# Kernel optimization log

Hardware: AMD Instinct MI355X
Metric: run time of the kernel (lower is better)

## Reference

```python
import jax, jax.numpy as jnp
import numpy as np

B, S, D = 4, 1024, 4096
HQ, HKV, HD = 32, 8, 128
N_REP = HQ // HKV


def _rope(x, cos, sin):
    # x: [b, s, h, hd]; cos/sin: [s, hd//2]; pairs are (x[..., 2i], x[..., 2i+1])
    xr = x[..., 0::2]
    xi = x[..., 1::2]
    c = cos[None, :, None, :]
    s = sin[None, :, None, :]
    out_r = xr * c - xi * s
    out_i = xr * s + xi * c
    return jnp.stack([out_r, out_i], axis=-1).reshape(x.shape)


def setup_inputs() -> dict:
    key = jax.random.key(0)
    ks = jax.random.split(key, 6)
    x = jax.random.normal(ks[0], (B, S, D), dtype=jnp.float32)
    wq = jax.random.normal(ks[1], (HQ * HD, D), dtype=jnp.float32) * 0.02
    wk = jax.random.normal(ks[2], (HKV * HD, D), dtype=jnp.float32) * 0.02
    wv = jax.random.normal(ks[3], (HKV * HD, D), dtype=jnp.float32) * 0.02
    wo = jax.random.normal(ks[4], (D, HQ * HD), dtype=jnp.float32) * 0.02
    # standard rotary frequencies, theta=10000
    inv_freq = 1.0 / (10000.0 ** (np.arange(0, HD, 2, dtype=np.float32) / HD))
    angles = np.outer(np.arange(S, dtype=np.float32), inv_freq)  # [S, HD//2]
    freqs_cos = jnp.asarray(np.cos(angles), dtype=jnp.float32)
    freqs_sin = jnp.asarray(np.sin(angles), dtype=jnp.float32)
    cache_k = jnp.zeros((B, S, HKV, HD), dtype=jnp.float32)
    cache_v = jnp.zeros((B, S, HKV, HD), dtype=jnp.float32)
    return {"x": x, "wq": wq, "wk": wk, "wv": wv, "wo": wo,
            "freqs_cos": freqs_cos, "freqs_sin": freqs_sin,
            "cache_k": cache_k, "cache_v": cache_v, "start_pos": 0}


def reference(x, wq, wk, wv, wo, freqs_cos, freqs_sin, cache_k, cache_v, start_pos):
    b, s, _ = x.shape
    xq = jnp.einsum('bsd,od->bso', x, wq).reshape(b, s, HQ, HD)
    xk = jnp.einsum('bsd,od->bso', x, wk).reshape(b, s, HKV, HD)
    xv = jnp.einsum('bsd,od->bso', x, wv).reshape(b, s, HKV, HD)
    xq = _rope(xq, freqs_cos, freqs_sin)
    xk = _rope(xk, freqs_cos, freqs_sin)
    # KV-cache append (intended semantics: store keys/values)
    cache_k = jax.lax.dynamic_update_slice(cache_k, xk, (0, start_pos, 0, 0))
    cache_v = jax.lax.dynamic_update_slice(cache_v, xv, (0, start_pos, 0, 0))
    keys = cache_k[:, :start_pos + s]      # [b, kv, HKV, HD]
    values = cache_v[:, :start_pos + s]
    # GQA repeat_kv -> [b, kv, HQ, HD]
    keys = jnp.repeat(keys, N_REP, axis=2)
    values = jnp.repeat(values, N_REP, axis=2)
    scores = jnp.einsum('bqhd,bkhd->bhqk', xq, keys) / jnp.sqrt(jnp.float32(HD))
    probs = jax.nn.softmax(scores.astype(jnp.float32), axis=-1).astype(xq.dtype)
    out = jnp.einsum('bhqk,bkhd->bqhd', probs, values).reshape(b, s, HQ * HD)
    return jnp.einsum('bso,do->bsd', out, wo)
```

## Files before the change

kernel.cpp:

```cpp
#include <hip/hip_runtime.h>

typedef __bf16 bf16_t;
typedef __bf16 bf16x8 __attribute__((ext_vector_type(8)));
typedef __bf16 bf16x4 __attribute__((ext_vector_type(4)));
typedef float  f32x4  __attribute__((ext_vector_type(4)));
typedef short  s16x4  __attribute__((ext_vector_type(4)));

#define SEQ    1024
#define DMODEL 4096
#define NHQ    32
#define NHKV   8
#define HDIM   128

#define GLOAD_LDS16(g, l)                                                  \
    __builtin_amdgcn_global_load_lds(                                      \
        (const __attribute__((address_space(1))) unsigned int*)(g),        \
        (__attribute__((address_space(3))) unsigned int*)(l), 16, 0, 0)

__global__ __launch_bounds__(256)
void f2b(const float* __restrict__ in, bf16_t* __restrict__ out, int n8)
{
    int i = blockIdx.x * 256 + threadIdx.x;
    if (i >= n8) return;
    const float4* p = (const float4*)in + 2 * (size_t)i;
    float4 a = p[0], b = p[1];
    bf16x8 o;
    o[0] = (bf16_t)a.x; o[1] = (bf16_t)a.y; o[2] = (bf16_t)a.z; o[3] = (bf16_t)a.w;
    o[4] = (bf16_t)b.x; o[5] = (bf16_t)b.y; o[6] = (bf16_t)b.z; o[7] = (bf16_t)b.w;
    *((bf16x8*)out + i) = o;
}

#define STAGE_A(b, ks)  do {                                               \
    const char* as_ = Ab + (size_t)srow * Krb + (ks) + scol0;              \
    GLOAD_LDS16(as_,             ldsA[b] + t * 16);                        \
    GLOAD_LDS16(as_ + 128 * Krb, ldsA[b] + 8192 + t * 16);                 \
} while (0)
#define STAGE_B(b, ks)  do {                                               \
    const char* bs_ = Bb + (size_t)srow * Krb + (ks) + scol0;              \
    GLOAD_LDS16(bs_,             ldsB[b] + t * 16);                        \
    GLOAD_LDS16(bs_ + 128 * Krb, ldsB[b] + 8192 + t * 16);                 \
} while (0)
#define LDS_AT(buf, row, lg_) \
    (*(const bf16x8*)((buf) + (row) * 64 + (((lg_) * 16) ^ ((((row) >> 1) & 3) << 4))))

#define TILE(bufi, tno)  do {                                              \
    const int ks3_ = ((tno) + 3 < NT) ? ((tno) + 3) * 64 : 0;              \
      \
    bf16x8 af[8], bfr0, bfr1;                                              \
    _Pragma("unroll")                                                      \
    for (int m = 0; m < 8; ++m) {                                          \
        int row = wm * 128 + m * 16 + l15;                                 \
        af[m] = LDS_AT(ldsA[bufi], row, lg);                               \
    }                                                                      \
    { int rb = wn * 64 + l15;      bfr0 = LDS_AT(ldsB[bufi], rb, lg); }    \
    { int rb = wn * 64 + 16 + l15; bfr1 = LDS_AT(ldsB[bufi], rb, lg); }    \
    STAGE_A(((tno) + 3) & 3, ks3_);                                        \
    __builtin_amdgcn_sched_barrier(0);                                     \
    __builtin_amdgcn_s_barrier();                                          \
    asm volatile("s_waitcnt lgkmcnt(0)" ::: "memory");                     \
    __builtin_amdgcn_sched_barrier(0);                                     \
    __builtin_amdgcn_s_setprio(1);                                         \
    _Pragma("unroll")                                                      \
    for (int m = 0; m < 8; ++m) {                                          \
        acc[m][0] = __builtin_amdgcn_mfma_f32_16x16x32_bf16(af[m], bfr0, acc[m][0], 0, 0, 0); \
        acc[m][1] = __builtin_amdgcn_mfma_f32_16x16x32_bf16(af[m], bfr1, acc[m][1], 0, 0, 0); \
    }                                                                      \
    __builtin_amdgcn_s_setprio(0);                                         \
    __builtin_amdgcn_sched_barrier(0);                                     \
    __builtin_amdgcn_s_barrier();                                          \
       \
    { int rb = wn * 64 + 32 + l15; bfr0 = LDS_AT(ldsB[bufi], rb, lg); }    \
    { int rb = wn * 64 + 48 + l15; bfr1 = LDS_AT(ldsB[bufi], rb, lg); }    \
    STAGE_B(((tno) + 3) & 3, ks3_);                                        \
    __builtin_amdgcn_sched_barrier(0);                                     \
    __builtin_amdgcn_s_barrier();                                          \
    asm volatile("s_waitcnt lgkmcnt(0)" ::: "memory");                     \
    __builtin_amdgcn_sched_barrier(0);                                     \
    __builtin_amdgcn_s_setprio(1);                                         \
    _Pragma("unroll")                                                      \
    for (int m = 0; m < 8; ++m) {                                          \
        acc[m][2] = __builtin_amdgcn_mfma_f32_16x16x32_bf16(af[m], bfr0, acc[m][2], 0, 0, 0); \
        acc[m][3] = __builtin_amdgcn_mfma_f32_16x16x32_bf16(af[m], bfr1, acc[m][3], 0, 0, 0); \
    }                                                                      \
    __builtin_amdgcn_s_setprio(0);                                         \
    asm volatile("s_waitcnt vmcnt(8)" ::: "memory");                       \
    __builtin_amdgcn_sched_barrier(0);                                     \
    __builtin_amdgcn_s_barrier();                                          \
} while (0)

template<bool OUT_F32>
__global__ __launch_bounds__(512, 2)
void gemm256(const bf16_t* __restrict__ A, const bf16_t* __restrict__ B,
             void* __restrict__ Cv, int M, int N, int K, int nbn)
{
    __shared__ __align__(16) char ldsA[4][16384];
    __shared__ __align__(16) char ldsB[4][16384];

    const int nwg = gridDim.x;
    const int bid0 = blockIdx.x;
    const int bid = (bid0 & 7) * (nwg >> 3) + (bid0 >> 3);
    const int bm = bid / nbn, bn = bid % nbn;
    const int t = threadIdx.x;
    const int lane = t & 63, wid = t >> 6;
    const int wm = wid >> 2, wn = wid & 3;
    const int l15 = lane & 15, lg = lane >> 4;
    const int m0 = bm * 256, n0 = bn * 256;

    const int srow = t >> 2;
    const int scol0 = (((t & 3) ^ ((srow >> 1) & 3)) << 4);
    const int Krb = K * 2;
    const char* Ab = (const char*)A + (size_t)m0 * Krb;
    const char* Bb = (const char*)B + (size_t)n0 * Krb;

    const int NT = K >> 5;
    f32x4 acc[8][4] = {};

    STAGE_A(0, 0);   STAGE_B(0, 0);
    STAGE_A(1, 64);  STAGE_B(1, 64);
    STAGE_A(2, 128); STAGE_B(2, 128);
    asm volatile("s_waitcnt vmcnt(8)" ::: "memory");
    __builtin_amdgcn_sched_barrier(0);
    __builtin_amdgcn_s_barrier();

    for (int tt = 0; tt < NT; tt += 4) {
        TILE(0, tt + 0);
        TILE(1, tt + 1);
        TILE(2, tt + 2);
        TILE(3, tt + 3);
    }

    #pragma unroll
    for (int m = 0; m < 8; ++m) {
        int row0 = m0 + wm * 128 + m * 16 + lg * 4;
        #pragma unroll
        for (int n = 0; n < 4; ++n) {
            int col = n0 + wn * 64 + n * 16 + l15;
            #pragma unroll
            for (int i = 0; i < 4; ++i) {
                if constexpr (OUT_F32)
                    ((float*)Cv)[(size_t)(row0 + i) * N + col] = acc[m][n][i];
                else
                    ((bf16_t*)Cv)[(size_t)(row0 + i) * N + col] = (bf16_t)acc[m][n][i];
            }
        }
    }
}
#undef TILE
#undef LDS_AT
#undef STAGE_A
#undef STAGE_B

template<int MODE>
__global__ __launch_bounds__(256, 4)
void gemm_bt(const bf16_t* __restrict__ A, const bf16_t* __restrict__ B,
             void* __restrict__ Cv, bf16_t* __restrict__ Vt,
             int M, int N, int K, int nbn)
{
    __shared__ __align__(16) bf16_t lA[128 * 32];
    __shared__ __align__(16) bf16_t lB[128 * 32];

    const int nwg = gridDim.x;
    const int bid0 = blockIdx.x;
    const int bid = (bid0 & 7) * (nwg >> 3) + (bid0 >> 3);
    const int bm = bid / nbn, bn = bid % nbn;
    const int t = threadIdx.x;
    const int lane = t & 63, wid = t >> 6;
    const int wrow = (wid >> 1) * 64, wcol = (wid & 1) * 64;
    const int l15 = lane & 15, lg = lane >> 4;
    const int m0 = bm * 128, n0 = bn * 128;

    const int r0 = t >> 2, pos0 = (t & 3) * 8;
    const int r1 = r0 + 64;

    const bf16_t* Ar0 = A + (size_t)(m0 + r0) * K + pos0;
    const bf16_t* Ar1 = A + (size_t)(m0 + r1) * K + pos0;
    const bf16_t* Br0 = B + (size_t)(n0 + r0) * K + pos0;
    const bf16_t* Br1 = B + (size_t)(n0 + r1) * K + pos0;

    f32x4 acc[4][4] = {};

    for (int k0 = 0; k0 < K; k0 += 32) {
        __syncthreads();
        GLOAD_LDS16(Ar0 + k0, lA + t * 8);
        GLOAD_LDS16(Ar1 + k0, lA + (t + 256) * 8);
        GLOAD_LDS16(Br0 + k0, lB + t * 8);
        GLOAD_LDS16(Br1 + k0, lB + (t + 256) * 8);
        __syncthreads();

        bf16x8 af[4], bfr[4];
        #pragma unroll
        for (int m = 0; m < 4; ++m)
            af[m] = *(const bf16x8*)(lA + (wrow + m * 16 + l15) * 32 + lg * 8);
        #pragma unroll
        for (int n = 0; n < 4; ++n)
            bfr[n] = *(const bf16x8*)(lB + (wcol + n * 16 + l15) * 32 + lg * 8);
        #pragma unroll
        for (int m = 0; m < 4; ++m)
            #pragma unroll
            for (int n = 0; n < 4; ++n)
                acc[m][n] = __builtin_amdgcn_mfma_f32_16x16x32_bf16(
                    af[m], bfr[n], acc[m][n], 0, 0, 0);
    }

    #pragma unroll
    for (int m = 0; m < 4; ++m) {
        #pragma unroll
        for (int n = 0; n < 4; ++n) {
            int col  = n0 + wcol + n * 16 + l15;
            int row0 = m0 + wrow + m * 16 + lg * 4;
            if constexpr (MODE == 0) {
                #pragma unroll
                for (int i = 0; i < 4; ++i)
                    ((bf16_t*)Cv)[(size_t)(row0 + i) * N + col] = (bf16_t)acc[m][n][i];
            } else if constexpr (MODE == 1) {
                #pragma unroll
                for (int i = 0; i < 4; ++i)
                    ((float*)Cv)[(size_t)(row0 + i) * N + col] = acc[m][n][i];
            } else {
                if (col < 1024) {
                    #pragma unroll
                    for (int i = 0; i < 4; ++i)
                        ((bf16_t*)Cv)[(size_t)(row0 + i) * 1024 + col] = (bf16_t)acc[m][n][i];
                } else {
                    bf16x4 pk;
                    #pragma unroll
                    for (int i = 0; i < 4; ++i) pk[i] = (bf16_t)acc[m][n][i];
                    *(bf16x4*)(Vt + (size_t)(col - 1024) * 4096 + row0) = pk;
                }
            }
        }
    }
}

__global__ __launch_bounds__(256)
void rope_kernel(bf16_t* __restrict__ X, const float* __restrict__ fc,
                 const float* __restrict__ fs, int nheads, int rowstride)
{
    int idx = blockIdx.x * 256 + threadIdx.x;
    int j4 = idx & 15;
    int rest = idx >> 4;
    int h = rest % nheads;
    int tok = rest / nheads;
    int s = tok & (SEQ - 1);
    bf16_t* p = X + (size_t)tok * rowstride + h * HDIM + j4 * 8;
    bf16x8 v = *(const bf16x8*)p;
    float4 c  = *(const float4*)(fc + s * 64 + j4 * 4);
    float4 sn = *(const float4*)(fs + s * 64 + j4 * 4);
    bf16x8 o;
    o[0] = (bf16_t)((float)v[0] * c.x - (float)v[1] * sn.x);
    o[1] = (bf16_t)((float)v[0] * sn.x + (float)v[1] * c.x);
    o[2] = (bf16_t)((float)v[2] * c.y - (float)v[3] * sn.y);
    o[3] = (bf16_t)((float)v[2] * sn.y + (float)v[3] * c.y);
    o[4] = (bf16_t)((float)v[4] * c.z - (float)v[5] * sn.z);
    o[5] = (bf16_t)((float)v[4] * sn.z + (float)v[5] * c.z);
    o[6] = (bf16_t)((float)v[6] * c.w - (float)v[7] * sn.w);
    o[7] = (bf16_t)((float)v[6] * sn.w + (float)v[7] * c.w);
    *(bf16x8*)p = o;
}

__global__ __launch_bounds__(256, 4)
void attn_kernel(const bf16_t* __restrict__ Q, const bf16_t* __restrict__ Kg,
                 const bf16_t* __restrict__ Vtg, bf16_t* __restrict__ O)
{
    __shared__ __align__(16) char klds[64 * 256];
    __shared__ __align__(16) char vlds[128 * 128];

    const int nwg = gridDim.x;
    const int bid0 = blockIdx.x;
    const int blk = (bid0 & 7) * (nwg >> 3) + (bid0 >> 3);
    const int qt = blk & 15;
    const int bh = blk >> 4;
    const int b = bh >> 5, h = bh & 31, kv = h >> 2;
    const int t = threadIdx.x, lane = t & 63, wid = t >> 6;
    const int l15 = lane & 15, lg = lane >> 4;
    const int swzk = (l15 & 7) << 4;

    const float SCL = 0.08838834764831845f;
    const float L2E = 1.4426950408889634f;

    const int qrow = qt * 64 + wid * 16 + l15;
    const size_t qbase = (size_t)(b * SEQ + qrow) * DMODEL + h * HDIM;
    bf16x8 qf[4];
    #pragma unroll
    for (int dc = 0; dc < 4; ++dc)
        qf[dc] = *(const bf16x8*)(Q + qbase + dc * 32 + lg * 8);

    const char* kgb = (const char*)Kg + ((size_t)(b * SEQ) * 1024 + kv * HDIM) * 2;
    const char* vgb = (const char*)Vtg + ((size_t)(kv * HDIM) * 4096 + b * SEQ) * 2;

    f32x4 o[8] = {};
    float mrun = -3.0e38f, lrun = 0.f;

    for (int kt = 0; kt < 16; ++kt) {
        __syncthreads();
        #pragma unroll
        for (int i = 0; i < 4; ++i) {
            int idx = t + 256 * i;
            {
                int r = idx >> 4, cb = (idx & 15) << 4;
                const char* src = kgb + (size_t)(kt * 64 + r) * 2048
                                      + (cb ^ ((r & 7) << 4));
                GLOAD_LDS16(src, klds + idx * 16);
            }
            {
                int d = idx >> 3, cb = (idx & 7) << 4;
                const char* src = vgb + (size_t)d * 8192 + kt * 128
                                      + (cb ^ ((d & 7) << 4));
                GLOAD_LDS16(src, vlds + idx * 16);
            }
        }
        __syncthreads();

        f32x4 sacc[4] = {};
        #pragma unroll
        for (int kb = 0; kb < 4; ++kb) {
            const char* krow = klds + (kb * 16 + l15) * 256;
            #pragma unroll
            for (int dc = 0; dc < 4; ++dc) {
                bf16x8 kf = *(const bf16x8*)(krow + ((dc * 64 + lg * 16) ^ swzk));
                sacc[kb] = __builtin_amdgcn_mfma_f32_16x16x32_bf16(
                    kf, qf[dc], sacc[kb], 0, 0, 0);
            }
        }

        float sv[16];
        float mt = -3.0e38f;
        #pragma unroll
        for (int kb = 0; kb < 4; ++kb)
            #pragma unroll
            for (int i = 0; i < 4; ++i) {
                float s = sacc[kb][i] * SCL;
                sv[kb * 4 + i] = s;
                mt = fmaxf(mt, s);
            }
        mt = fmaxf(mt, __shfl_xor(mt, 16));
        mt = fmaxf(mt, __shfl_xor(mt, 32));
        float mnew = fmaxf(mrun, mt);
        float alpha = exp2f((mrun - mnew) * L2E);

        float ts = 0.f;
        s16x4 pf[4];
        #pragma unroll
        for (int kb = 0; kb < 4; ++kb)
            #pragma unroll
            for (int i = 0; i < 4; ++i) {
                float p = exp2f((sv[kb * 4 + i] - mnew) * L2E);
                ts += p;
                pf[kb][i] = (short)__builtin_bit_cast(unsigned short, (bf16_t)p);
            }
        ts += __shfl_xor(ts, 16);
        ts += __shfl_xor(ts, 32);
        lrun = lrun * alpha + ts;
        mrun = mnew;

        #pragma unroll
        for (int i = 0; i < 4; ++i) {
            float ai = __shfl(alpha, lg * 4 + i);
            #pragma unroll
            for (int db = 0; db < 8; ++db) o[db][i] *= ai;
        }

        #pragma unroll
        for (int kb = 0; kb < 4; ++kb)
            #pragma unroll
            for (int db = 0; db < 8; ++db) {
                int d = l15 + 16 * db;
                const char* va = vlds + d * 128 + ((kb * 32 + lg * 8) ^ swzk);
                s16x4 vf = *(const s16x4*)va;
                o[db] = __builtin_amdgcn_mfma_f32_16x16x16bf16_1k(
                    pf[kb], vf, o[db], 0, 0, 0);
            }
    }

    #pragma unroll
    for (int i = 0; i < 4; ++i) {
        float li = __shfl(lrun, lg * 4 + i);
        float inv = 1.0f / li;
        int row = b * SEQ + qt * 64 + wid * 16 + lg * 4 + i;
        #pragma unroll
        for (int db = 0; db < 8; ++db) {
            int col = h * HDIM + l15 + 16 * db;
            O[(size_t)row * DMODEL + col] = (bf16_t)(o[db][i] * inv);
        }
    }
}

extern "C" void kernel_launch(void* const* d_in, const int* in_sizes, int n_in,
                              void* d_out, int out_size, void* d_ws, size_t ws_size,
                              hipStream_t stream)
{
    const float* x  = (const float*)d_in[0];
    const float* wq = (const float*)d_in[1];
    const float* wk = (const float*)d_in[2];
    const float* wv = (const float*)d_in[3];
    const float* wo = (const float*)d_in[4];
    const float* fc = (const float*)d_in[5];
    const float* fs = (const float*)d_in[6];

    const size_t T = (size_t)4096;
    bf16_t* Qw   = (bf16_t*)d_ws;
    bf16_t* Kw2  = Qw   + T * 4096;
    bf16_t* Vt   = Kw2  + T * 1024;
    bf16_t* AO   = Vt   + T * 1024;
    bf16_t* xb   = AO   + T * 4096;
    bf16_t* wqb  = xb   + T * 4096;
    bf16_t* wkvb = wqb  + T * 4096;
    bf16_t* wob  = wkvb + T * 2048;

    f2b<<<8192, 256, 0, stream>>>(x,  xb,  4096 * 4096 / 8);
    f2b<<<8192, 256, 0, stream>>>(wq, wqb, 4096 * 4096 / 8);
    f2b<<<2048, 256, 0, stream>>>(wk, wkvb,                       1024 * 4096 / 8);
    f2b<<<2048, 256, 0, stream>>>(wv, wkvb + (size_t)1024 * 4096, 1024 * 4096 / 8);
    f2b<<<8192, 256, 0, stream>>>(wo, wob, 4096 * 4096 / 8);

    gemm256<false><<<256, 512, 0, stream>>>(xb, wqb, Qw, 4096, 4096, 4096, 16);
    gemm_bt<2><<<512, 256, 0, stream>>>(xb, wkvb, Kw2, Vt, 4096, 2048, 4096, 16);

    rope_kernel<<<8192, 256, 0, stream>>>(Qw,  fc, fs, NHQ,  4096);
    rope_kernel<<<2048, 256, 0, stream>>>(Kw2, fc, fs, NHKV, 1024);

    attn_kernel<<<2048, 256, 0, stream>>>(Qw, Kw2, Vt, AO);

    gemm256<true><<<256, 512, 0, stream>>>(AO, wob, d_out, 4096, 4096, 4096, 16);
}
```

Baseline: 563.9 us.

## Merge GEMM tile phases, fold softmax scale into RoPE, add lazy rescaling

The GEMM tile loop now loads all four B fragments at once, issues both A and B staging together, and runs all 32 MFMAs in one phase, which halves the workgroup barriers per k-tile. The softmax scale 1/sqrt(HD) is folded into the Q RoPE multiply so the attention kernel drops the per-score multiply. The attention kernel also skips the running-max update and the output rescale unless some lane's tile max exceeds the running max by more than 8. This threshold trick lets probabilities exceed 1 and trades some numerical headroom for fewer exp and shuffle operations. Removing one barrier per phase changes the LDS buffer reuse ordering, which risks races when a buffer is restaged while others still read it.

```diff
diff --git a/kernel.cpp b/kernel.cpp
--- a/kernel.cpp
+++ b/kernel.cpp
@@ -45,47 +45,31 @@
 
 #define TILE(bufi, tno)  do {                                              \
     const int ks3_ = ((tno) + 3 < NT) ? ((tno) + 3) * 64 : 0;              \
-      \
-    bf16x8 af[8], bfr0, bfr1;                                              \
+    __builtin_amdgcn_s_barrier();              \
+    __builtin_amdgcn_sched_barrier(0);                                     \
+    bf16x8 af[8], bf0, bf1, bf2, bf3;                                      \
     _Pragma("unroll")                                                      \
-    for (int m = 0; m < 8; ++m) {                                          \
-        int row = wm * 128 + m * 16 + l15;                                 \
-        af[m] = LDS_AT(ldsA[bufi], row, lg);                               \
-    }                                                                      \
-    { int rb = wn * 64 + l15;      bfr0 = LDS_AT(ldsB[bufi], rb, lg); }    \
-    { int rb = wn * 64 + 16 + l15; bfr1 = LDS_AT(ldsB[bufi], rb, lg); }    \
+    for (int m = 0; m < 8; ++m)                                            \
+        af[m] = LDS_AT(ldsA[bufi], wm * 128 + m * 16 + l15, lg);           \
+    bf0 = LDS_AT(ldsB[bufi], wn * 64 +  0 + l15, lg);                      \
+    bf1 = LDS_AT(ldsB[bufi], wn * 64 + 16 + l15, lg);                      \
+    bf2 = LDS_AT(ldsB[bufi], wn * 64 + 32 + l15, lg);                      \
+    bf3 = LDS_AT(ldsB[bufi], wn * 64 + 48 + l15, lg);                      \
     STAGE_A(((tno) + 3) & 3, ks3_);                                        \
-    __builtin_amdgcn_sched_barrier(0);                                     \
-    __builtin_amdgcn_s_barrier();                                          \
+    STAGE_B(((tno) + 3) & 3, ks3_);                                        \
     asm volatile("s_waitcnt lgkmcnt(0)" ::: "memory");                     \
     __builtin_amdgcn_sched_barrier(0);                                     \
     __builtin_amdgcn_s_setprio(1);                                         \
     _Pragma("unroll")                                                      \
     for (int m = 0; m < 8; ++m) {                                          \
-        acc[m][0] = __builtin_amdgcn_mfma_f32_16x16x32_bf16(af[m], bfr0, acc[m][0], 0, 0, 0); \
-        acc[m][1] = __builtin_amdgcn_mfma_f32_16x16x32_bf16(af[m], bfr1, acc[m][1], 0, 0, 0); \
+        acc[m][0] = __builtin_amdgcn_mfma_f32_16x16x32_bf16(af[m], bf0, acc[m][0], 0, 0, 0); \
+        acc[m][1] = __builtin_amdgcn_mfma_f32_16x16x32_bf16(af[m], bf1, acc[m][1], 0, 0, 0); \
+        acc[m][2] = __builtin_amdgcn_mfma_f32_16x16x32_bf16(af[m], bf2, acc[m][2], 0, 0, 0); \
+        acc[m][3] = __builtin_amdgcn_mfma_f32_16x16x32_bf16(af[m], bf3, acc[m][3], 0, 0, 0); \
     }                                                                      \
     __builtin_amdgcn_s_setprio(0);                                         \
+    asm volatile("s_waitcnt vmcnt(8)" ::: "memory");       \
     __builtin_amdgcn_sched_barrier(0);                                     \
-    __builtin_amdgcn_s_barrier();                                          \
-       \
-    { int rb = wn * 64 + 32 + l15; bfr0 = LDS_AT(ldsB[bufi], rb, lg); }    \
-    { int rb = wn * 64 + 48 + l15; bfr1 = LDS_AT(ldsB[bufi], rb, lg); }    \
-    STAGE_B(((tno) + 3) & 3, ks3_);                                        \
-    __builtin_amdgcn_sched_barrier(0);                                     \
-    __builtin_amdgcn_s_barrier();                                          \
-    asm volatile("s_waitcnt lgkmcnt(0)" ::: "memory");                     \
-    __builtin_amdgcn_sched_barrier(0);                                     \
-    __builtin_amdgcn_s_setprio(1);                                         \
-    _Pragma("unroll")                                                      \
-    for (int m = 0; m < 8; ++m) {                                          \
-        acc[m][2] = __builtin_amdgcn_mfma_f32_16x16x32_bf16(af[m], bfr0, acc[m][2], 0, 0, 0); \
-        acc[m][3] = __builtin_amdgcn_mfma_f32_16x16x32_bf16(af[m], bfr1, acc[m][3], 0, 0, 0); \
-    }                                                                      \
-    __builtin_amdgcn_s_setprio(0);                                         \
-    asm volatile("s_waitcnt vmcnt(8)" ::: "memory");                       \
-    __builtin_amdgcn_sched_barrier(0);                                     \
-    __builtin_amdgcn_s_barrier();                                          \
 } while (0)
 
 template<bool OUT_F32>
@@ -120,7 +104,6 @@
     STAGE_A(2, 128); STAGE_B(2, 128);
     asm volatile("s_waitcnt vmcnt(8)" ::: "memory");
     __builtin_amdgcn_sched_barrier(0);
-    __builtin_amdgcn_s_barrier();
 
     for (int tt = 0; tt < NT; tt += 4) {
         TILE(0, tt + 0);
@@ -234,7 +217,8 @@
 
 __global__ __launch_bounds__(256)
 void rope_kernel(bf16_t* __restrict__ X, const float* __restrict__ fc,
-                 const float* __restrict__ fs, int nheads, int rowstride)
+                 const float* __restrict__ fs, int nheads, int rowstride,
+                 float oscale)
 {
     int idx = blockIdx.x * 256 + threadIdx.x;
     int j4 = idx & 15;
@@ -246,6 +230,8 @@
     bf16x8 v = *(const bf16x8*)p;
     float4 c  = *(const float4*)(fc + s * 64 + j4 * 4);
     float4 sn = *(const float4*)(fs + s * 64 + j4 * 4);
+    c.x *= oscale; c.y *= oscale; c.z *= oscale; c.w *= oscale;
+    sn.x *= oscale; sn.y *= oscale; sn.z *= oscale; sn.w *= oscale;
     bf16x8 o;
     o[0] = (bf16_t)((float)v[0] * c.x - (float)v[1] * sn.x);
     o[1] = (bf16_t)((float)v[0] * sn.x + (float)v[1] * c.x);
@@ -275,7 +261,6 @@
     const int l15 = lane & 15, lg = lane >> 4;
     const int swzk = (l15 & 7) << 4;
 
-    const float SCL = 0.08838834764831845f;
     const float L2E = 1.4426950408889634f;
 
     const int qrow = qt * 64 + wid * 16 + l15;
@@ -329,35 +314,48 @@
         for (int kb = 0; kb < 4; ++kb)
             #pragma unroll
             for (int i = 0; i < 4; ++i) {
-                float s = sacc[kb][i] * SCL;
+                float s = sacc[kb][i];
                 sv[kb * 4 + i] = s;
                 mt = fmaxf(mt, s);
             }
         mt = fmaxf(mt, __shfl_xor(mt, 16));
         mt = fmaxf(mt, __shfl_xor(mt, 32));
-        float mnew = fmaxf(mrun, mt);
-        float alpha = exp2f((mrun - mnew) * L2E);
 
         float ts = 0.f;
         s16x4 pf[4];
-        #pragma unroll
-        for (int kb = 0; kb < 4; ++kb)
+        if (__any(mt > mrun + 8.0f)) {
+            float mnew = fmaxf(mrun, mt);
+            float alpha = exp2f((mrun - mnew) * L2E);
+            #pragma unroll
+            for (int kb = 0; kb < 4; ++kb)
+                #pragma unroll
+                for (int i = 0; i < 4; ++i) {
+                    float p = exp2f((sv[kb * 4 + i] - mnew) * L2E);
+                    ts += p;
+                    pf[kb][i] = (short)__builtin_bit_cast(unsigned short, (bf16_t)p);
+                }
+            ts += __shfl_xor(ts, 16);
+            ts += __shfl_xor(ts, 32);
+            lrun = lrun * alpha + ts;
+            mrun = mnew;
             #pragma unroll
             for (int i = 0; i < 4; ++i) {
-                float p = exp2f((sv[kb * 4 + i] - mnew) * L2E);
-                ts += p;
-                pf[kb][i] = (short)__builtin_bit_cast(unsigned short, (bf16_t)p);
-            }
-        ts += __shfl_xor(ts, 16);
-        ts += __shfl_xor(ts, 32);
-        lrun = lrun * alpha + ts;
-        mrun = mnew;
-
-        #pragma unroll
-        for (int i = 0; i < 4; ++i) {
-            float ai = __shfl(alpha, lg * 4 + i);
-            #pragma unroll
-            for (int db = 0; db < 8; ++db) o[db][i] *= ai;
+                float ai = __shfl(alpha, lg * 4 + i);
+                #pragma unroll
+                for (int db = 0; db < 8; ++db) o[db][i] *= ai;
+            }
+        } else {
+            #pragma unroll
+            for (int kb = 0; kb < 4; ++kb)
+                #pragma unroll
+                for (int i = 0; i < 4; ++i) {
+                    float p = exp2f((sv[kb * 4 + i] - mrun) * L2E);
+                    ts += p;
+                    pf[kb][i] = (short)__builtin_bit_cast(unsigned short, (bf16_t)p);
+                }
+            ts += __shfl_xor(ts, 16);
+            ts += __shfl_xor(ts, 32);
+            lrun += ts;
         }
 
         #pragma unroll
@@ -416,8 +414,9 @@
     gemm256<false><<<256, 512, 0, stream>>>(xb, wqb, Qw, 4096, 4096, 4096, 16);
     gemm_bt<2><<<512, 256, 0, stream>>>(xb, wkvb, Kw2, Vt, 4096, 2048, 4096, 16);
 
-    rope_kernel<<<8192, 256, 0, stream>>>(Qw,  fc, fs, NHQ,  4096);
-    rope_kernel<<<2048, 256, 0, stream>>>(Kw2, fc, fs, NHKV, 1024);
+    rope_kernel<<<8192, 256, 0, stream>>>(Qw,  fc, fs, NHQ,  4096,
+                                          0.08838834764831845f);
+    rope_kernel<<<2048, 256, 0, stream>>>(Kw2, fc, fs, NHKV, 1024, 1.0f);
 
     attn_kernel<<<2048, 256, 0, stream>>>(Qw, Kw2, Vt, AO);
 
```

After: 598.6 us. 1.06x slower.
